# Kernel tuning notes

Measured on AMD Instinct MI355X. Metric: run time of the kernel, lower is better.

Reference implementation:

```python
import jax, jax.numpy as jnp
import numpy as np

DIM = 1024
HEADS = 16
HEAD_DIM = DIM // HEADS


def rotate_half(x):
    x1, x2 = jnp.split(x, 2, axis=-1)
    return jnp.concatenate((-x2, x1), axis=-1)


def rope_tables(T, D, dtype=jnp.float32):
    inv_freq = 1.0 / (10000.0 ** (jnp.arange(0, D, 2, dtype=jnp.float32) / D))
    t = jnp.arange(T, dtype=jnp.float32)
    freqs = jnp.einsum('i,j->ij', t, inv_freq)  # [T, D/2]
    emb = jnp.concatenate((freqs, freqs), axis=-1)  # [T, D]
    return emb.astype(dtype), jnp.cos(emb).astype(dtype), jnp.sin(emb).astype(dtype)


def setup_inputs() -> dict:
    key = jax.random.key(0)
    kx, kq, kk, kv, ko = jax.random.split(key, 5)
    B, T = 2, 4096
    scale = 1.0 / np.sqrt(DIM)
    x = jax.random.normal(kx, (B, T, DIM), dtype=jnp.float32)
    wq = jax.random.normal(kq, (DIM, DIM), dtype=jnp.float32) * scale
    wk = jax.random.normal(kk, (DIM, DIM), dtype=jnp.float32) * scale
    wv = jax.random.normal(kv, (DIM, DIM), dtype=jnp.float32) * scale
    wo = jax.random.normal(ko, (DIM, DIM), dtype=jnp.float32) * scale
    return {"x": x, "wq": wq, "wk": wk, "wv": wv, "wo": wo}


def reference(x, wq, wk, wv, wo):
    B, T, C = x.shape
    H, D = HEADS, HEAD_DIM
    # projections; nn.Linear applies x @ W^T
    q = (x @ wq.T).reshape(B, T, H, D).transpose(0, 2, 1, 3)  # [B,H,T,D]
    k = (x @ wk.T).reshape(B, T, H, D).transpose(0, 2, 1, 3)
    v = (x @ wv.T).reshape(B, T, H, D).transpose(0, 2, 1, 3)
    _, cos, sin = rope_tables(T, D, x.dtype)
    cos = cos[None, None]  # [1,1,T,D]
    sin = sin[None, None]
    q = q * cos + rotate_half(q) * sin
    k = k * cos + rotate_half(k) * sin
    scores = jnp.einsum('bhtd,bhsd->bhts', q, k) / jnp.sqrt(jnp.asarray(D, x.dtype))
    attn = jax.nn.softmax(scores, axis=-1)
    out = jnp.einsum('bhts,bhsd->bhtd', attn, v)
    out = out.transpose(0, 2, 1, 3).reshape(B, T, C)
    return out @ wo.T
```

## Files before the change

kernel.cpp:

```cpp
#include <hip/hip_runtime.h>
#include <hip/hip_bf16.h>
#include <math.h>


typedef __attribute__((ext_vector_type(8))) short short8;
typedef __attribute__((ext_vector_type(4))) short short4v;
typedef __attribute__((ext_vector_type(4))) float floatx4;

using bf16 = __hip_bfloat16;

static constexpr int T_ = 4096;
static constexpr int C_ = 1024;
static constexpr int M_ = 8192;
static constexpr float QSCALE = 0.125f * 1.44269504088896340736f;

#if __has_builtin(__builtin_amdgcn_mfma_f32_16x16x16bf16_1k)
#define USE_K16 1
#else
#define USE_K16 0
#endif

#if __has_builtin(__builtin_amdgcn_exp2f)
#define EXP2 __builtin_amdgcn_exp2f
#else
#define EXP2 exp2f
#endif

__device__ __forceinline__ floatx4 mfma16(short8 a, short8 b, floatx4 c) {
    return __builtin_amdgcn_mfma_f32_16x16x32_bf16(a, b, c, 0, 0, 0);
}
#if USE_K16
__device__ __forceinline__ floatx4 mfma_k16(short4v a, short4v b, floatx4 c) {
    return __builtin_amdgcn_mfma_f32_16x16x16bf16_1k(a, b, c, 0, 0, 0);
}
#endif

__device__ __forceinline__ short8 ld8(const bf16* p) {
    return *reinterpret_cast<const short8*>(p);
}
__device__ __forceinline__ short4v ld4(const bf16* p) {
    return *reinterpret_cast<const short4v*>(p);
}
__device__ __forceinline__ void st8(bf16* p, short8 v) {
    *reinterpret_cast<short8*>(p) = v;
}
__device__ __forceinline__ unsigned short f2bf(float x) {
    bf16 h = __float2bfloat16(x);
    return reinterpret_cast<unsigned short&>(h);
}

__device__ __forceinline__ int pack2bf(float a, float b, unsigned sel) {
    const unsigned ua = __float_as_uint(a) + 0x8000u;
    const unsigned ub = __float_as_uint(b) + 0x8000u;
    int r;
    asm("v_perm_b32 %0, %1, %2, %3" : "=v"(r) : "v"(ub), "v"(ua), "s"(sel));
    return r;
}
__device__ __forceinline__ short4v i2s4(int lo, int hi) {
    union { int2 i; short4v s; } u;
    u.i.x = lo; u.i.y = hi;
    return u.s;
}
__device__ __forceinline__ short8 i2s8(int a, int b, int c, int d) {
    union { int4 i; short8 s; } u;
    u.i.x = a; u.i.y = b; u.i.z = c; u.i.w = d;
    return u.s;
}

__device__ __forceinline__ void cp16(const bf16* g, bf16* l) {
    __builtin_amdgcn_global_load_lds(
        (const __attribute__((address_space(1))) void*)g,
        (__attribute__((address_space(3))) void*)l, 16, 0, 0);
}

__global__ __launch_bounds__(256)
void cvt_kernel(const float* __restrict__ in, bf16* __restrict__ out, int n8) {
    const int i = blockIdx.x * blockDim.x + threadIdx.x;
    if (i >= n8) return;
    const float4* p = reinterpret_cast<const float4*>(in) + (size_t)i * 2;
    const float4 a = p[0];
    const float4 b = p[1];
    short8 v;
    v[0] = (short)f2bf(a.x); v[1] = (short)f2bf(a.y);
    v[2] = (short)f2bf(a.z); v[3] = (short)f2bf(a.w);
    v[4] = (short)f2bf(b.x); v[5] = (short)f2bf(b.y);
    v[6] = (short)f2bf(b.z); v[7] = (short)f2bf(b.w);
    *(reinterpret_cast<short8*>(out) + i) = v;
}

__global__ __launch_bounds__(256)
void gemm128_kernel(const bf16* __restrict__ A, const bf16* __restrict__ W,
                    void* __restrict__ out, int mode) {
    const int m0   = blockIdx.x * 128;
    const int n0   = blockIdx.y * 128;
    const int tid  = threadIdx.x;
    const int lane = tid & 63;
    const int wave = tid >> 6;
    const int quad = lane >> 4;
    const int lr   = lane & 15;
    const int wr   = (wave >> 1) * 64;
    const int wc   = (wave & 1) * 64;

    __shared__ __align__(16) bf16 Als[2][128 * 32];
    __shared__ __align__(16) bf16 Bls[2][128 * 32];

    const int srow = tid >> 2;
    const int scol = (tid & 3) * 8;

    floatx4 acc[4][4];
#pragma unroll
    for (int i = 0; i < 4; ++i)
#pragma unroll
        for (int j = 0; j < 4; ++j) acc[i][j] = floatx4{0.f, 0.f, 0.f, 0.f};

    const bf16* Ab = A + (size_t)m0 * C_;
    const bf16* Wb = W + (size_t)n0 * C_;

#pragma unroll
    for (int j = 0; j < 2; ++j) {
        const int row = srow + j * 64;
        cp16(Ab + (size_t)row * C_ + scol, &Als[0][(j * 256 + tid) * 8]);
        cp16(Wb + (size_t)row * C_ + scol, &Bls[0][(j * 256 + tid) * 8]);
    }
    __syncthreads();

    for (int k = 0; k < C_; k += 32) {
        const int buf = (k >> 5) & 1;
        if (k + 32 < C_) {
            const int nb = buf ^ 1;
#pragma unroll
            for (int j = 0; j < 2; ++j) {
                const int row = srow + j * 64;
                cp16(Ab + (size_t)row * C_ + k + 32 + scol,
                     &Als[nb][(j * 256 + tid) * 8]);
                cp16(Wb + (size_t)row * C_ + k + 32 + scol,
                     &Bls[nb][(j * 256 + tid) * 8]);
            }
        }

        short8 a[4], b[4];
#pragma unroll
        for (int i = 0; i < 4; ++i)
            a[i] = ld8(&Als[buf][(wr + i * 16 + lr) * 32 + quad * 8]);
#pragma unroll
        for (int j = 0; j < 4; ++j)
            b[j] = ld8(&Bls[buf][(wc + j * 16 + lr) * 32 + quad * 8]);
#pragma unroll
        for (int i = 0; i < 4; ++i)
#pragma unroll
            for (int j = 0; j < 4; ++j) acc[i][j] = mfma16(a[i], b[j], acc[i][j]);

        __syncthreads();
    }

    if (mode == 0) {
        bf16* ob = (bf16*)out;
#pragma unroll
        for (int j = 0; j < 4; ++j) {
            const int col = n0 + wc + j * 16 + lr;
#pragma unroll
            for (int i = 0; i < 4; ++i)
#pragma unroll
                for (int r = 0; r < 4; ++r) {
                    const int m = m0 + wr + i * 16 + quad * 4 + r;
                    ob[(size_t)m * C_ + col] = __float2bfloat16(acc[i][j][r]);
                }
        }
    } else if (mode == 1) {
        unsigned short* ob = (unsigned short*)out;
        const int b2 = m0 >> 12;
#pragma unroll
        for (int j = 0; j < 4; ++j) {
            const int n = n0 + wc + j * 16 + lr;
            const int h = n >> 6;
            const int d = n & 63;
#pragma unroll
            for (int i = 0; i < 4; ++i) {
                const int t0 = (m0 & 4095) + wr + i * 16 + quad * 4;
                ushort4 v;
                v.x = f2bf(acc[i][j][0]); v.y = f2bf(acc[i][j][1]);
                v.z = f2bf(acc[i][j][2]); v.w = f2bf(acc[i][j][3]);
                size_t idx = ((size_t)((b2 * 16 + h) * 64 + d)) * T_ + t0;
                *reinterpret_cast<ushort4*>(ob + idx) = v;
            }
        }
    } else {
        float* of = (float*)out;
#pragma unroll
        for (int j = 0; j < 4; ++j) {
            const int col = n0 + wc + j * 16 + lr;
#pragma unroll
            for (int i = 0; i < 4; ++i)
#pragma unroll
                for (int r = 0; r < 4; ++r) {
                    const int m = m0 + wr + i * 16 + quad * 4 + r;
                    of[(size_t)m * C_ + col] = acc[i][j][r];
                }
        }
    }
}

__global__ __launch_bounds__(256)
void gemm_qkv_kernel(const bf16* __restrict__ A, const bf16* __restrict__ W,
                     bf16* __restrict__ Qbase) {
    const int m0   = blockIdx.x * 128;
    const int n0g  = blockIdx.y * 128;
    const int tid  = threadIdx.x;
    const int lane = tid & 63;
    const int wave = tid >> 6;
    const int quad = lane >> 4;
    const int lr   = lane & 15;
    const int wr   = (wave >> 1) * 64;
    const int wc   = (wave & 1) * 64;

    __shared__ __align__(16) bf16 Als[2][128 * 32];
    __shared__ __align__(16) bf16 Bls[2][128 * 32];

    const int srow = tid >> 2;
    const int scol = (tid & 3) * 8;

    floatx4 acc[4][4];
#pragma unroll
    for (int i = 0; i < 4; ++i)
#pragma unroll
        for (int j = 0; j < 4; ++j) acc[i][j] = floatx4{0.f, 0.f, 0.f, 0.f};

    const bf16* Ab = A + (size_t)m0 * C_;
    const bf16* Wb = W + (size_t)n0g * C_;

#pragma unroll
    for (int j = 0; j < 2; ++j) {
        const int row = srow + j * 64;
        cp16(Ab + (size_t)row * C_ + scol, &Als[0][(j * 256 + tid) * 8]);
        cp16(Wb + (size_t)row * C_ + scol, &Bls[0][(j * 256 + tid) * 8]);
    }
    __syncthreads();

    for (int k = 0; k < C_; k += 32) {
        const int buf = (k >> 5) & 1;
        if (k + 32 < C_) {
            const int nb = buf ^ 1;
#pragma unroll
            for (int j = 0; j < 2; ++j) {
                const int row = srow + j * 64;
                cp16(Ab + (size_t)row * C_ + k + 32 + scol,
                     &Als[nb][(j * 256 + tid) * 8]);
                cp16(Wb + (size_t)row * C_ + k + 32 + scol,
                     &Bls[nb][(j * 256 + tid) * 8]);
            }
        }

        short8 a[4], b[4];
#pragma unroll
        for (int i = 0; i < 4; ++i)
            a[i] = ld8(&Als[buf][(wr + i * 16 + lr) * 32 + quad * 8]);
#pragma unroll
        for (int j = 0; j < 4; ++j)
            b[j] = ld8(&Bls[buf][(wc + j * 16 + lr) * 32 + quad * 8]);
#pragma unroll
        for (int i = 0; i < 4; ++i)
#pragma unroll
            for (int j = 0; j < 4; ++j) acc[i][j] = mfma16(a[i], b[j], acc[i][j]);

        __syncthreads();
    }

    const int seg = n0g >> 10;
    const int n0  = n0g & 1023;
    if (seg < 2) {
        bf16* ob = Qbase + (size_t)seg * M_ * C_;
#pragma unroll
        for (int j = 0; j < 4; ++j) {
            const int col = n0 + wc + j * 16 + lr;
#pragma unroll
            for (int i = 0; i < 4; ++i)
#pragma unroll
                for (int r = 0; r < 4; ++r) {
                    const int m = m0 + wr + i * 16 + quad * 4 + r;
                    ob[(size_t)m * C_ + col] = __float2bfloat16(acc[i][j][r]);
                }
        }
    } else {
        unsigned short* ob = (unsigned short*)(Qbase + (size_t)2 * M_ * C_);
        const int b2 = m0 >> 12;
#pragma unroll
        for (int j = 0; j < 4; ++j) {
            const int n = n0 + wc + j * 16 + lr;
            const int h = n >> 6;
            const int d = n & 63;
#pragma unroll
            for (int i = 0; i < 4; ++i) {
                const int t0 = (m0 & 4095) + wr + i * 16 + quad * 4;
                ushort4 v;
                v.x = f2bf(acc[i][j][0]); v.y = f2bf(acc[i][j][1]);
                v.z = f2bf(acc[i][j][2]); v.w = f2bf(acc[i][j][3]);
                size_t idx = ((size_t)((b2 * 16 + h) * 64 + d)) * T_ + t0;
                *reinterpret_cast<ushort4*>(ob + idx) = v;
            }
        }
    }
}

__global__ __launch_bounds__(256)
void rope_kernel(bf16* __restrict__ Q, bf16* __restrict__ K) {
    const int tid  = blockIdx.x * blockDim.x + threadIdx.x;
    const int m    = tid >> 9;
    const int rest = tid & 511;
    const int h    = rest >> 5;
    const int j    = rest & 31;
    const int t    = m & 4095;

    const float inv_freq = expf(-(float)j * 0.28782313662425575f);
    const float angle = (float)t * inv_freq;
    float s, c;
    sincosf(angle, &s, &c);

    const size_t base = (size_t)m * C_ + h * 64 + j;

    float q1 = __bfloat162float(Q[base]);
    float q2 = __bfloat162float(Q[base + 32]);
    Q[base]      = __float2bfloat16((q1 * c - q2 * s) * QSCALE);
    Q[base + 32] = __float2bfloat16((q2 * c + q1 * s) * QSCALE);

    float k1 = __bfloat162float(K[base]);
    float k2 = __bfloat162float(K[base + 32]);
    K[base]      = __float2bfloat16(k1 * c - k2 * s);
    K[base + 32] = __float2bfloat16(k2 * c + k1 * s);
}

__global__ __launch_bounds__(256)
void attn_kernel(const bf16* __restrict__ Q, const bf16* __restrict__ K,
                 const bf16* __restrict__ Vt, bf16* __restrict__ AO) {
    const int tid  = threadIdx.x;
    const int lane = tid & 63;
    const int wave = tid >> 6;
    const int quad = lane >> 4;
    const int lr   = lane & 15;
    const int bh   = blockIdx.y;
    const int b    = bh >> 4;
    const int h    = bh & 15;
    const int q0   = blockIdx.x * 128 + wave * 32;

    const bf16* Qb = Q + (size_t)b * T_ * C_ + h * 64;
    const bf16* Kb = K + (size_t)b * T_ * C_ + h * 64;
    const bf16* Vb = Vt + (size_t)bh * 64 * T_;

#if USE_K16
    __shared__ __align__(16) bf16 Kls[2][64 * 64];
    __shared__ __align__(16) bf16 Vls[2][64 * 64];

    const int srow  = tid >> 3;
    const int sc    = tid & 7;
    const int sphys = (sc ^ (srow & 7)) * 8;
    const int soff0 = srow * 64 + sphys;
    const int soff1 = (srow + 32) * 64 + sphys;

    const unsigned psel = 0x07060302u;
    const floatx4 FZ = {0.f, 0.f, 0.f, 0.f};
    const int one2 = 0x3F803F80;
    const short8 VONE = i2s8(one2, one2, one2, one2);

    short8 aq[2][2];
#pragma unroll
    for (int t = 0; t < 2; ++t) {
        aq[t][0] = ld8(Qb + (size_t)(q0 + t * 16 + lr) * C_ + quad * 8);
        aq[t][1] = ld8(Qb + (size_t)(q0 + t * 16 + lr) * C_ + 32 + quad * 8);
    }

    floatx4 O[2][4];
#pragma unroll
    for (int t = 0; t < 2; ++t)
#pragma unroll
        for (int dt = 0; dt < 4; ++dt) O[t][dt] = floatx4{0.f, 0.f, 0.f, 0.f};
    floatx4 Osum[2] = {{0.f, 0.f, 0.f, 0.f}, {0.f, 0.f, 0.f, 0.f}};

    const int lr7    = lr & 7;
    const int kchunk = (quad ^ lr7) * 8;
    const int vsub   = (quad & 1) * 4;
    const int vbq    = quad >> 1;
    const int kel0   = lr * 64 + kchunk;
    const int kel1   = kel0 ^ 32;
    int velk[4];
#pragma unroll
    for (int kk = 0; kk < 4; ++kk)
        velk[kk] = lr * 64 + (((2 * kk + vbq) ^ lr7) * 8) + vsub;

    short8 kr0, kr1, vr0, vr1;
#define LOAD_STAGE(kv0)                                              \
    do {                                                             \
        kr0 = ld8(Kb + (size_t)((kv0) + srow) * C_ + sc * 8);        \
        kr1 = ld8(Kb + (size_t)((kv0) + srow + 32) * C_ + sc * 8);   \
        vr0 = ld8(Vb + (size_t)srow * T_ + (kv0) + sc * 8);          \
        vr1 = ld8(Vb + (size_t)(srow + 32) * T_ + (kv0) + sc * 8);   \
    } while (0)
#define STORE_STAGE(p)                                               \
    do {                                                             \
        st8(&Kls[p][soff0], kr0);                                    \
        st8(&Kls[p][soff1], kr1);                                    \
        st8(&Vls[p][soff0], vr0);                                    \
        st8(&Vls[p][soff1], vr1);                                    \
    } while (0)

#define BAR()                                                        \
    do {                                                             \
        asm volatile("s_waitcnt lgkmcnt(0)" ::: "memory");           \
        __builtin_amdgcn_s_barrier();                                \
    } while (0)

#define COMPUTE(P)                                                            \
    do {                                                                      \
        const bf16* Ks = Kls[P];                                              \
        const bf16* Vs = Vls[P];                                              \
        int prlo[2][4], prhi[2][4];                                           \
        _Pragma("unroll")                                                     \
        for (int kk = 0; kk < 4; ++kk) {                                      \
            const short8 kf0 = ld8(Ks + kk * 1024 + kel0);                    \
            const short8 kf1 = ld8(Ks + kk * 1024 + kel1);                    \
            floatx4 s0 = mfma16(kf0, aq[0][0], FZ);                           \
            s0 = mfma16(kf1, aq[0][1], s0);                                   \
            floatx4 s1 = mfma16(kf0, aq[1][0], FZ);                           \
            s1 = mfma16(kf1, aq[1][1], s1);                                   \
            const float e0 = EXP2(s0[0]), e1 = EXP2(s0[1]);                   \
            const float e2 = EXP2(s0[2]), e3 = EXP2(s0[3]);                   \
            prlo[0][kk] = pack2bf(e0, e1, psel);                              \
            prhi[0][kk] = pack2bf(e2, e3, psel);                              \
            const float f0 = EXP2(s1[0]), f1 = EXP2(s1[1]);                   \
            const float f2 = EXP2(s1[2]), f3 = EXP2(s1[3]);                   \
            prlo[1][kk] = pack2bf(f0, f1, psel);                              \
            prhi[1][kk] = pack2bf(f2, f3, psel);                              \
        }                                                                     \
        \
        Osum[0] = mfma16(i2s8(prlo[0][0], prhi[0][0], prlo[0][1], prhi[0][1]),\
                         VONE, Osum[0]);                                      \
        Osum[0] = mfma16(i2s8(prlo[0][2], prhi[0][2], prlo[0][3], prhi[0][3]),\
                         VONE, Osum[0]);                                      \
        Osum[1] = mfma16(i2s8(prlo[1][0], prhi[1][0], prlo[1][1], prhi[1][1]),\
                         VONE, Osum[1]);                                      \
        Osum[1] = mfma16(i2s8(prlo[1][2], prhi[1][2], prlo[1][3], prhi[1][3]),\
                         VONE, Osum[1]);                                      \
        __builtin_amdgcn_s_setprio(1);                                        \
        _Pragma("unroll")                                                     \
        for (int dt = 0; dt < 4; ++dt) {                                      \
            _Pragma("unroll")                                                 \
            for (int kk = 0; kk < 4; ++kk) {                                  \
                const short4v vf = ld4(Vs + dt * 1024 + velk[kk]);            \
                O[0][dt] = mfma_k16(i2s4(prlo[0][kk], prhi[0][kk]), vf, O[0][dt]); \
                O[1][dt] = mfma_k16(i2s4(prlo[1][kk], prhi[1][kk]), vf, O[1][dt]); \
            }                                                                 \
        }                                                                     \
        __builtin_amdgcn_s_setprio(0);                                        \
    } while (0)

    LOAD_STAGE(0);
    STORE_STAGE(0);
    LOAD_STAGE(64);
    BAR();

    constexpr int NS = T_ / 64;
    for (int s = 0; s < NS; s += 2) {
        if (s + 1 < NS) STORE_STAGE(1);
        if (s + 2 < NS) LOAD_STAGE((s + 2) * 64);
        COMPUTE(0);
        BAR();
        if (s + 2 < NS) STORE_STAGE(0);
        if (s + 3 < NS) LOAD_STAGE((s + 3) * 64);
        COMPUTE(1);
        BAR();
    }

#pragma unroll
    for (int t = 0; t < 2; ++t) {
#pragma unroll
        for (int r = 0; r < 4; ++r) {
            const float inv = 1.0f / fmaxf(Osum[t][r], 1e-30f);
            const size_t row =
                (size_t)(b * T_ + q0 + t * 16 + quad * 4 + r) * C_ + h * 64;
            AO[row + 0  + lr] = __float2bfloat16(O[t][0][r] * inv);
            AO[row + 16 + lr] = __float2bfloat16(O[t][1][r] * inv);
            AO[row + 32 + lr] = __float2bfloat16(O[t][2][r] * inv);
            AO[row + 48 + lr] = __float2bfloat16(O[t][3][r] * inv);
        }
    }
#undef LOAD_STAGE
#undef STORE_STAGE
#undef COMPUTE
#undef BAR
#else
    __shared__ __align__(16) unsigned short Pbuf[4][512];
    unsigned short* Pw = Pbuf[wave];
    for (int half = 0; half < 2; ++half) {
        const int qh = q0 + half * 16;
        const short8 aq0 = ld8(Qb + (size_t)(qh + lr) * C_ + quad * 8);
        const short8 aq1 = ld8(Qb + (size_t)(qh + lr) * C_ + 32 + quad * 8);
        floatx4 O0 = {0,0,0,0}, O1 = {0,0,0,0}, O2 = {0,0,0,0}, O3 = {0,0,0,0};
        float lrun[4] = {0.f, 0.f, 0.f, 0.f};
        for (int kv = 0; kv < T_; kv += 32) {
            floatx4 S0 = {0,0,0,0}, S1 = {0,0,0,0};
            const bf16* k0 = Kb + (size_t)(kv + lr) * C_ + quad * 8;
            const bf16* k1 = Kb + (size_t)(kv + 16 + lr) * C_ + quad * 8;
            S0 = mfma16(aq0, ld8(k0), S0);
            S0 = mfma16(aq1, ld8(k0 + 32), S0);
            S1 = mfma16(aq0, ld8(k1), S1);
            S1 = mfma16(aq1, ld8(k1 + 32), S1);
#pragma unroll
            for (int r = 0; r < 4; ++r) {
                const float e0 = exp2f(S0[r]);
                const float e1 = exp2f(S1[r]);
                lrun[r] += e0 + e1;
                const int row = quad * 4 + r;
                Pw[row * 32 + lr]      = f2bf(e0);
                Pw[row * 32 + 16 + lr] = f2bf(e1);
            }
            __syncthreads();
            const short8 ap = *reinterpret_cast<const short8*>(Pw + lr * 32 + quad * 8);
            O0 = mfma16(ap, ld8(Vb + (size_t)(lr)      * T_ + kv + quad * 8), O0);
            O1 = mfma16(ap, ld8(Vb + (size_t)(16 + lr) * T_ + kv + quad * 8), O1);
            O2 = mfma16(ap, ld8(Vb + (size_t)(32 + lr) * T_ + kv + quad * 8), O2);
            O3 = mfma16(ap, ld8(Vb + (size_t)(48 + lr) * T_ + kv + quad * 8), O3);
            __syncthreads();
        }
#pragma unroll
        for (int r = 0; r < 4; ++r) {
            float l = lrun[r];
            l += __shfl_xor(l, 1); l += __shfl_xor(l, 2);
            l += __shfl_xor(l, 4); l += __shfl_xor(l, 8);
            const float inv = 1.0f / fmaxf(l, 1e-30f);
            const size_t row = (size_t)(b * T_ + qh + quad * 4 + r) * C_ + h * 64;
            AO[row + 0  + lr] = __float2bfloat16(O0[r] * inv);
            AO[row + 16 + lr] = __float2bfloat16(O1[r] * inv);
            AO[row + 32 + lr] = __float2bfloat16(O2[r] * inv);
            AO[row + 48 + lr] = __float2bfloat16(O3[r] * inv);
        }
    }
#endif
}

extern "C" void kernel_launch(void* const* d_in, const int* in_sizes, int n_in,
                              void* d_out, int out_size, void* d_ws, size_t ws_size,
                              hipStream_t stream) {
    const float* x  = (const float*)d_in[0];
    const float* wq = (const float*)d_in[1];
    const float* wk = (const float*)d_in[2];
    const float* wv = (const float*)d_in[3];
    const float* wo = (const float*)d_in[4];
    float* out = (float*)d_out;

    bf16* xb  = (bf16*)d_ws;
    bf16* wqb = xb  + (size_t)M_ * C_;
    bf16* wkb = wqb + (size_t)C_ * C_;
    bf16* wvb = wkb + (size_t)C_ * C_;
    bf16* wob = wvb + (size_t)C_ * C_;
    bf16* Q   = wob + (size_t)C_ * C_;
    bf16* K   = Q   + (size_t)M_ * C_;
    bf16* Vt  = K   + (size_t)M_ * C_;
    bf16* AO  = xb;

    cvt_kernel<<<(M_ * C_ / 8 + 255) / 256, 256, 0, stream>>>(x, xb, M_ * C_ / 8);
    cvt_kernel<<<(C_ * C_ / 8 + 255) / 256, 256, 0, stream>>>(wq, wqb, C_ * C_ / 8);
    cvt_kernel<<<(C_ * C_ / 8 + 255) / 256, 256, 0, stream>>>(wk, wkb, C_ * C_ / 8);
    cvt_kernel<<<(C_ * C_ / 8 + 255) / 256, 256, 0, stream>>>(wv, wvb, C_ * C_ / 8);
    cvt_kernel<<<(C_ * C_ / 8 + 255) / 256, 256, 0, stream>>>(wo, wob, C_ * C_ / 8);

    gemm_qkv_kernel<<<dim3(M_ / 128, 24), dim3(256), 0, stream>>>(xb, wqb, Q);

    rope_kernel<<<(M_ * 512) / 256, 256, 0, stream>>>(Q, K);

    attn_kernel<<<dim3(T_ / 128, 32), 256, 0, stream>>>(Q, K, Vt, AO);

    gemm128_kernel<<<dim3(M_ / 128, C_ / 128), dim3(256), 0, stream>>>(AO, wob, out, 2);
}
```

Baseline: 391.6 us.

## Fuse RoPE into QKV GEMM epilogue and batch weight conversions

Moves the rotary embedding and Q scaling into the QKV GEMM epilogue, so Q and K no longer make a separate bf16 read-modify-write pass. The rotation uses a precomputed cos/sin table, which relies on each 64-column wave tile covering one whole head so both halves are in registers. The four weight conversions are merged into one launch and the rope kernel is removed. The cost is a per-element table load in the epilogue and extra workspace for the table.

```diff
diff --git a/kernel.cpp b/kernel.cpp
--- a/kernel.cpp
+++ b/kernel.cpp
@@ -89,6 +89,36 @@
 }
 
 __global__ __launch_bounds__(256)
+void cvt4_kernel(const float* __restrict__ p0, const float* __restrict__ p1,
+                 const float* __restrict__ p2, const float* __restrict__ p3,
+                 bf16* __restrict__ out) {
+    const int i   = blockIdx.x * blockDim.x + threadIdx.x;
+    const int seg = i >> 17;
+    const int off = i & 131071;
+    const float* in = (seg == 0) ? p0 : (seg == 1) ? p1 : (seg == 2) ? p2 : p3;
+    const float4* p = reinterpret_cast<const float4*>(in) + (size_t)off * 2;
+    const float4 a = p[0];
+    const float4 b = p[1];
+    short8 v;
+    v[0] = (short)f2bf(a.x); v[1] = (short)f2bf(a.y);
+    v[2] = (short)f2bf(a.z); v[3] = (short)f2bf(a.w);
+    v[4] = (short)f2bf(b.x); v[5] = (short)f2bf(b.y);
+    v[6] = (short)f2bf(b.z); v[7] = (short)f2bf(b.w);
+    *(reinterpret_cast<short8*>(out) + i) = v;
+}
+
+__global__ __launch_bounds__(256)
+void rope_table_kernel(float2* __restrict__ CS) {
+    const int i = blockIdx.x * blockDim.x + threadIdx.x;
+    const int t = i >> 5;
+    const int j = i & 31;
+    const float inv_freq = expf(-(float)j * 0.28782313662425575f);
+    float s, c;
+    sincosf((float)t * inv_freq, &s, &c);
+    CS[i] = make_float2(c, s);
+}
+
+__global__ __launch_bounds__(256)
 void gemm128_kernel(const bf16* __restrict__ A, const bf16* __restrict__ W,
                     void* __restrict__ out, int mode) {
     const int m0   = blockIdx.x * 128;
@@ -202,7 +232,7 @@
 
 __global__ __launch_bounds__(256)
 void gemm_qkv_kernel(const bf16* __restrict__ A, const bf16* __restrict__ W,
-                     bf16* __restrict__ Qbase) {
+                     bf16* __restrict__ Qbase, const float2* __restrict__ CS) {
     const int m0   = blockIdx.x * 128;
     const int n0g  = blockIdx.y * 128;
     const int tid  = threadIdx.x;
@@ -269,16 +299,27 @@
     const int n0  = n0g & 1023;
     if (seg < 2) {
         bf16* ob = Qbase + (size_t)seg * M_ * C_;
-#pragma unroll
-        for (int j = 0; j < 4; ++j) {
-            const int col = n0 + wc + j * 16 + lr;
-#pragma unroll
-            for (int i = 0; i < 4; ++i)
+        const float scale = (seg == 0) ? QSCALE : 1.0f;
+        const int tb = (m0 & 4095) + wr + quad * 4;
+#pragma unroll
+        for (int j = 0; j < 2; ++j) {
+            const int col  = n0 + wc + j * 16 + lr;
+            const int jcol = j * 16 + lr;
+#pragma unroll
+            for (int i = 0; i < 4; ++i) {
 #pragma unroll
                 for (int r = 0; r < 4; ++r) {
+                    const int t = tb + i * 16 + r;
+                    const float2 cs = CS[t * 32 + jcol];
+                    const float q1 = acc[i][j][r];
+                    const float q2 = acc[i][j + 2][r];
                     const int m = m0 + wr + i * 16 + quad * 4 + r;
-                    ob[(size_t)m * C_ + col] = __float2bfloat16(acc[i][j][r]);
+                    ob[(size_t)m * C_ + col] =
+                        __float2bfloat16((q1 * cs.x - q2 * cs.y) * scale);
+                    ob[(size_t)m * C_ + col + 32] =
+                        __float2bfloat16((q2 * cs.x + q1 * cs.y) * scale);
                 }
+            }
         }
     } else {
         unsigned short* ob = (unsigned short*)(Qbase + (size_t)2 * M_ * C_);
@@ -299,33 +340,6 @@
             }
         }
     }
-}
-
-__global__ __launch_bounds__(256)
-void rope_kernel(bf16* __restrict__ Q, bf16* __restrict__ K) {
-    const int tid  = blockIdx.x * blockDim.x + threadIdx.x;
-    const int m    = tid >> 9;
-    const int rest = tid & 511;
-    const int h    = rest >> 5;
-    const int j    = rest & 31;
-    const int t    = m & 4095;
-
-    const float inv_freq = expf(-(float)j * 0.28782313662425575f);
-    const float angle = (float)t * inv_freq;
-    float s, c;
-    sincosf(angle, &s, &c);
-
-    const size_t base = (size_t)m * C_ + h * 64 + j;
-
-    float q1 = __bfloat162float(Q[base]);
-    float q2 = __bfloat162float(Q[base + 32]);
-    Q[base]      = __float2bfloat16((q1 * c - q2 * s) * QSCALE);
-    Q[base + 32] = __float2bfloat16((q2 * c + q1 * s) * QSCALE);
-
-    float k1 = __bfloat162float(K[base]);
-    float k2 = __bfloat162float(K[base + 32]);
-    K[base]      = __float2bfloat16(k1 * c - k2 * s);
-    K[base + 32] = __float2bfloat16(k2 * c + k1 * s);
 }
 
 __global__ __launch_bounds__(256)
@@ -553,17 +567,14 @@
     bf16* Q   = wob + (size_t)C_ * C_;
     bf16* K   = Q   + (size_t)M_ * C_;
     bf16* Vt  = K   + (size_t)M_ * C_;
+    float2* CS = (float2*)(Vt + (size_t)M_ * C_);
     bf16* AO  = xb;
 
+    rope_table_kernel<<<(T_ * 32) / 256, 256, 0, stream>>>(CS);
     cvt_kernel<<<(M_ * C_ / 8 + 255) / 256, 256, 0, stream>>>(x, xb, M_ * C_ / 8);
-    cvt_kernel<<<(C_ * C_ / 8 + 255) / 256, 256, 0, stream>>>(wq, wqb, C_ * C_ / 8);
-    cvt_kernel<<<(C_ * C_ / 8 + 255) / 256, 256, 0, stream>>>(wk, wkb, C_ * C_ / 8);
-    cvt_kernel<<<(C_ * C_ / 8 + 255) / 256, 256, 0, stream>>>(wv, wvb, C_ * C_ / 8);
-    cvt_kernel<<<(C_ * C_ / 8 + 255) / 256, 256, 0, stream>>>(wo, wob, C_ * C_ / 8);
-
-    gemm_qkv_kernel<<<dim3(M_ / 128, 24), dim3(256), 0, stream>>>(xb, wqb, Q);
-
-    rope_kernel<<<(M_ * 512) / 256, 256, 0, stream>>>(Q, K);
+    cvt4_kernel<<<(4 * C_ * C_ / 8) / 256, 256, 0, stream>>>(wq, wk, wv, wo, wqb);
+
+    gemm_qkv_kernel<<<dim3(M_ / 128, 24), dim3(256), 0, stream>>>(xb, wqb, Q, CS);
 
     attn_kernel<<<dim3(T_ / 128, 32), 256, 0, stream>>>(Q, K, Vt, AO);
 
```

Result: no change. 393.1 us (+0.4%).
